# Kernel optimization log

Measured on AMD Instinct MI355X. Metric: run time of the kernel, lower is better.

The kernel has to match this reference:

```python
import jax, jax.numpy as jnp
import numpy as np
from jax import lax

V, H = 50257, 256
B, S, T = 128, 50, 32
TQ = 32


def position_encoding(emb):
    # emb: (B, S, T, H); l[s, e] = 1 - s/(T-1) - e/(H-1)*(1 - 2*s/(T-1))
    slen, elen = emb.shape[2], emb.shape[3]
    s = jnp.arange(slen, dtype=jnp.float32)[:, None] / (slen - 1)
    e = jnp.arange(elen, dtype=jnp.float32)[None, :] / (elen - 1)
    l = 1.0 - s - e * (1.0 - 2.0 * s)  # (T, H)
    return jnp.sum(emb * l[None, None], axis=2)  # (B, S, H)


def gru_seq(x, Wih, Whh, bih, bhh):
    # x: (B, T, H); torch GRU cell math; returns outputs (B,T,H), last hidden (B,H)
    h0 = jnp.zeros((x.shape[0], Whh.shape[1]), x.dtype)
    def step(h, xt):
        gi = xt @ Wih.T + bih
        gh = h @ Whh.T + bhh
        ir, iz, inn = jnp.split(gi, 3, axis=-1)
        hr, hz, hn = jnp.split(gh, 3, axis=-1)
        r = jax.nn.sigmoid(ir + hr)
        z = jax.nn.sigmoid(iz + hz)
        n = jnp.tanh(inn + r * hn)
        h_new = (1.0 - z) * n + z * h
        return h_new, h_new
    h_last, ys = lax.scan(step, h0, jnp.swapaxes(x, 0, 1))
    return jnp.swapaxes(ys, 0, 1), h_last


def setup_inputs() -> dict:
    key = jax.random.key(0)
    ks = jax.random.split(key, 16)
    def g(k, shape, scale=0.05):
        return (jax.random.normal(k, shape, dtype=jnp.float32) * scale)
    inp = {
        "contexts": jax.random.randint(ks[0], (B, S, T), 0, V, dtype=jnp.int32),
        "questions": jax.random.randint(ks[1], (B, TQ), 0, V, dtype=jnp.int32),
        "emb": jax.random.uniform(ks[2], (V, H), jnp.float32, -1.0, 1.0),
        "Wih_f": g(ks[3], (3 * H, H)), "Whh_f": g(ks[4], (3 * H, H)),
        "bih_f": jnp.zeros((3 * H,), jnp.float32), "bhh_f": jnp.zeros((3 * H,), jnp.float32),
        "Wih_b": g(ks[5], (3 * H, H)), "Whh_b": g(ks[6], (3 * H, H)),
        "bih_b": jnp.zeros((3 * H,), jnp.float32), "bhh_b": jnp.zeros((3 * H,), jnp.float32),
        "Wih_q": g(ks[7], (3 * H, H)), "Whh_q": g(ks[8], (3 * H, H)),
        "bih_q": jnp.zeros((3 * H,), jnp.float32), "bhh_q": jnp.zeros((3 * H,), jnp.float32),
        "Wo": g(ks[9], (V, H)), "bo": jnp.zeros((V,), jnp.float32),
    }
    return inp


def reference(contexts, questions, emb, Wih_f, Whh_f, bih_f, bhh_f,
              Wih_b, Whh_b, bih_b, bhh_b, Wih_q, Whh_q, bih_q, bhh_q, Wo, bo):
    # InputNet: embed -> position encoding -> bidirectional GRU (halves summed)
    ctx = emb[contexts]                      # (B, S, T, H)
    ctx = position_encoding(ctx)             # (B, S, H)  (dropout = eval no-op)
    out_f, _ = gru_seq(ctx, Wih_f, Whh_f, bih_f, bhh_f)
    out_b, _ = gru_seq(ctx[:, ::-1], Wih_b, Whh_b, bih_b, bhh_b)
    facts = out_f + out_b[:, ::-1]           # (B, S, H)
    # QuestionNet: embed -> GRU, take last hidden
    qemb = emb[questions]                    # (B, TQ, H)
    _, q = gru_seq(qemb, Wih_q, Whh_q, bih_q, bhh_q)   # (B, H)
    # AttnNet: dot-product scores + softmax over sentences (vectorized)
    energies = jnp.einsum('bsd,bd->bs', facts, q)
    attn = jax.nn.softmax(energies, axis=-1)           # (B, S)
    # memory read: bmm(attn, facts)
    read = jnp.einsum('bs,bsd->bd', attn, facts)       # (B, H)
    out = jnp.tanh(q * read) @ Wo.T + bo               # (B, V)
    return out
```

## Files before the change

### kernel.cpp

```cpp
#include <hip/hip_runtime.h>

#define V 50257
#define H 256
#define B 128
#define S 50
#define T 32
#define TQ 32

typedef __bf16 bf16x8 __attribute__((ext_vector_type(8)));
typedef float f32x4 __attribute__((ext_vector_type(4)));

__device__ inline unsigned short f2bf(float x) {
  __bf16 b = (__bf16)x;
  return __builtin_bit_cast(unsigned short, b);
}

__global__ __launch_bounds__(256) void k_wconv(
    const float* w0, const float* w1, const float* w2,
    const float* w3, const float* w4, const float* w5,
    unsigned short* dst) {
  int mat = blockIdx.x / 192;
  int blk = blockIdx.x % 192;
  const float* src = (mat == 0) ? w0 : (mat == 1) ? w1 : (mat == 2) ? w2
                   : (mat == 3) ? w3 : (mat == 4) ? w4 : w5;
  int off = blk * 1024 + threadIdx.x * 4;
  float4 v = *(const float4*)(src + off);
  unsigned short* d = dst + mat * 196608 + off;
  d[0] = f2bf(v.x); d[1] = f2bf(v.y); d[2] = f2bf(v.z); d[3] = f2bf(v.w);
}

__global__ __launch_bounds__(256) void k_embed(
    const int* ctx_idx, const int* q_idx, const float* emb,
    unsigned short* ctx_bf, unsigned short* q_bf) {
  __shared__ int sidx[T];
  int r = blockIdx.x;
  int tid = threadIdx.x;
  if (r < B * S) {
    if (tid < T) sidx[tid] = ctx_idx[r * T + tid];
    __syncthreads();
    float e = tid * (1.0f / 255.0f);
    float acc = 0.f;
    #pragma unroll 4
    for (int t = 0; t < T; ++t) {
      float tf = t * (1.0f / 31.0f);
      float w = (1.0f - tf) - e * (1.0f - 2.0f * tf);
      acc += emb[sidx[t] * H + tid] * w;
    }
    ctx_bf[r * H + tid] = f2bf(acc);
  } else {
    int rq = r - B * S;
    q_bf[rq * H + tid] = f2bf(emb[q_idx[rq] * H + tid]);
  }
}

__global__ __launch_bounds__(256) void k_gemm(
    const unsigned short* __restrict__ Xb, const unsigned short* __restrict__ Wb,
    const float* __restrict__ bias, float* __restrict__ Out) {
  const int n0 = blockIdx.x * 64;
  const int m0 = blockIdx.y * 128;
  __shared__ unsigned short lA[128 * 40];
  __shared__ unsigned short lB[64 * 40];
  int tid = threadIdx.x;
  int lane = tid & 63, wv = tid >> 6;
  int lr = lane & 15, lg = lane >> 4;
  f32x4 acc[2][4] = {};
  int sr = tid >> 2, skk = (tid & 3) * 8;
  for (int kt = 0; kt < 8; ++kt) {
    int k0 = kt * 32;
    __syncthreads();
    *(uint4*)&lA[sr * 40 + skk]        = *(const uint4*)&Xb[(m0 + sr) * 256 + k0 + skk];
    *(uint4*)&lA[(sr + 64) * 40 + skk] = *(const uint4*)&Xb[(m0 + sr + 64) * 256 + k0 + skk];
    *(uint4*)&lB[sr * 40 + skk]        = *(const uint4*)&Wb[(n0 + sr) * 256 + k0 + skk];
    __syncthreads();
    bf16x8 av0 = *(const bf16x8*)&lA[(wv * 32 + lr) * 40 + lg * 8];
    bf16x8 av1 = *(const bf16x8*)&lA[(wv * 32 + 16 + lr) * 40 + lg * 8];
    #pragma unroll
    for (int nt = 0; nt < 4; ++nt) {
      bf16x8 bv = *(const bf16x8*)&lB[(nt * 16 + lr) * 40 + lg * 8];
      acc[0][nt] = __builtin_amdgcn_mfma_f32_16x16x32_bf16(av0, bv, acc[0][nt], 0, 0, 0);
      acc[1][nt] = __builtin_amdgcn_mfma_f32_16x16x32_bf16(av1, bv, acc[1][nt], 0, 0, 0);
    }
  }
  #pragma unroll
  for (int nt = 0; nt < 4; ++nt) {
    int col = n0 + nt * 16 + lr;
    float bs = bias[col];
    #pragma unroll
    for (int mt = 0; mt < 2; ++mt) {
      #pragma unroll
      for (int r = 0; r < 4; ++r) {
        int row = m0 + wv * 32 + mt * 16 + lg * 4 + r;
        Out[row * 768 + col] = acc[mt][nt][r] + bs;
      }
    }
  }
}

__global__ __launch_bounds__(512) void k_rnn(
    const float* __restrict__ Gf, const float* __restrict__ Gb, const float* __restrict__ Gq,
    const unsigned short* __restrict__ WhF, const unsigned short* __restrict__ WhB,
    const unsigned short* __restrict__ WhQ,
    const float* __restrict__ bhF, const float* __restrict__ bhB, const float* __restrict__ bhQ,
    float* __restrict__ outF, float* __restrict__ outB, float* __restrict__ qvec) {
  int blk = blockIdx.x;
  int mode = blk >> 3;
  int rg = blk & 7;
  const float* G = (mode == 0) ? Gf : (mode == 1) ? Gb : Gq;
  const unsigned short* Wh = (mode == 0) ? WhF : (mode == 1) ? WhB : WhQ;
  const float* bh = (mode == 0) ? bhF : (mode == 1) ? bhB : bhQ;
  const int Tn = (mode == 2) ? TQ : S;
  const int SEQ = (mode == 2) ? TQ : S;
  float* ob = (mode == 0) ? outF : outB;

  __shared__ unsigned short hb[16 * 264];
  __shared__ float hf[16 * 264];

  int tid = threadIdx.x;
  for (int i = tid; i < 16 * 264; i += 512) { hb[i] = 0; hf[i] = 0.f; }
  int lane = tid & 63, wv = tid >> 6;
  int wcol = wv * 32;
  int lr = lane & 15, lg = lane >> 4;
  __syncthreads();

  for (int t = 0; t < Tn; ++t) {
    int s = (mode == 1) ? (S - 1 - t) : t;
    bf16x8 af[8];
    #pragma unroll
    for (int kt = 0; kt < 8; ++kt)
      af[kt] = *(const bf16x8*)&hb[lr * 264 + kt * 32 + lg * 8];
    __syncthreads();

    f32x4 acc[6] = {};
    #pragma unroll
    for (int g = 0; g < 3; ++g) {
      #pragma unroll
      for (int nt = 0; nt < 2; ++nt) {
        int n = g * 256 + wcol + nt * 16 + lr;
        const unsigned short* wp = Wh + n * 256 + lg * 8;
        #pragma unroll
        for (int kt = 0; kt < 8; ++kt) {
          bf16x8 bv = *(const bf16x8*)(wp + kt * 32);
          acc[g * 2 + nt] = __builtin_amdgcn_mfma_f32_16x16x32_bf16(af[kt], bv, acc[g * 2 + nt], 0, 0, 0);
        }
      }
    }
    #pragma unroll
    for (int nt = 0; nt < 2; ++nt) {
      int j = wcol + nt * 16 + lr;
      float bhr = bh[j], bhz = bh[256 + j], bhn = bh[512 + j];
      #pragma unroll
      for (int r = 0; r < 4; ++r) {
        int m = lg * 4 + r;
        int grow = ((rg * 16 + m) * SEQ + s) * 768;
        float xr = G[grow + j];
        float xz = G[grow + 256 + j];
        float xn = G[grow + 512 + j];
        float hr = acc[0 + nt][r] + bhr;
        float hz = acc[2 + nt][r] + bhz;
        float hn = acc[4 + nt][r] + bhn;
        float rgate = 1.f / (1.f + expf(-(xr + hr)));
        float zgate = 1.f / (1.f + expf(-(xz + hz)));
        float ngate = tanhf(xn + rgate * hn);
        float hold = hf[m * 264 + j];
        float hnew = (1.f - zgate) * ngate + zgate * hold;
        hf[m * 264 + j] = hnew;
        hb[m * 264 + j] = f2bf(hnew);
        if (mode == 2) {
          if (t == TQ - 1) qvec[(rg * 16 + m) * H + j] = hnew;
        } else {
          ob[((rg * 16 + m) * S + s) * H + j] = hnew;
        }
      }
    }
    __syncthreads();
  }
}

__global__ __launch_bounds__(256) void k_attn(
    const float* __restrict__ outF, const float* __restrict__ outB,
    const float* __restrict__ qvec, unsigned short* __restrict__ tqv) {
  int b = blockIdx.x, tid = threadIdx.x;
  __shared__ float fs[S * H];
  __shared__ float qs[H];
  __shared__ float es[S];
  qs[tid] = qvec[b * H + tid];
  for (int s = 0; s < S; ++s)
    fs[s * H + tid] = outF[(b * S + s) * H + tid] + outB[(b * S + s) * H + tid];
  __syncthreads();
  int lane = tid & 63, wv = tid >> 6;
  for (int s = wv; s < S; s += 4) {
    const float* fr = &fs[s * H];
    float p = 0.f;
    #pragma unroll
    for (int j = 0; j < 4; ++j) p += fr[lane * 4 + j] * qs[lane * 4 + j];
    #pragma unroll
    for (int off = 32; off > 0; off >>= 1) p += __shfl_xor(p, off, 64);
    if (lane == 0) es[s] = p;
  }
  __syncthreads();
  float mx = -1e30f;
  for (int s = 0; s < S; ++s) mx = fmaxf(mx, es[s]);
  float sum = 0.f;
  for (int s = 0; s < S; ++s) sum += expf(es[s] - mx);
  float inv = 1.f / sum;
  float rd = 0.f;
  for (int s = 0; s < S; ++s) rd += expf(es[s] - mx) * inv * fs[s * H + tid];
  tqv[b * H + tid] = f2bf(tanhf(qs[tid] * rd));
}

__global__ __launch_bounds__(256) void k_out(
    const unsigned short* __restrict__ tqv, const float* __restrict__ Wo,
    const float* __restrict__ bo, float* __restrict__ Out) {
  int n0 = blockIdx.x * 64;
  int tid = threadIdx.x, lane = tid & 63, wv = tid >> 6;
  int lr = lane & 15, lg = lane >> 4;
  __shared__ unsigned short lA[B * H];
  #pragma unroll
  for (int i = 0; i < 16; ++i) {
    int c = tid + i * 256;
    int row = c >> 5, kk = (c & 31) * 8;
    int dst = row * 512 + ((kk * 2) ^ ((row & 7) << 4));
    *(uint4*)((char*)lA + dst) = *(const uint4*)&tqv[row * H + kk];
  }
  __syncthreads();
  int vcol = n0 + wv * 16 + lr;
  int vc = (vcol < V) ? vcol : (V - 1);
  f32x4 acc[8] = {};
  for (int kt = 0; kt < 8; ++kt) {
    const float* wp = &Wo[vc * H + kt * 32 + lg * 8];
    float4 w0 = *(const float4*)wp;
    float4 w1 = *(const float4*)(wp + 4);
    bf16x8 bv;
    bv[0] = (__bf16)w0.x; bv[1] = (__bf16)w0.y; bv[2] = (__bf16)w0.z; bv[3] = (__bf16)w0.w;
    bv[4] = (__bf16)w1.x; bv[5] = (__bf16)w1.y; bv[6] = (__bf16)w1.z; bv[7] = (__bf16)w1.w;
    #pragma unroll
    for (int mt = 0; mt < 8; ++mt) {
      int row = mt * 16 + lr;
      int boff = row * 512 + ((kt * 64 + lg * 16) ^ ((row & 7) << 4));
      bf16x8 av = *(const bf16x8*)((const char*)lA + boff);
      acc[mt] = __builtin_amdgcn_mfma_f32_16x16x32_bf16(av, bv, acc[mt], 0, 0, 0);
    }
  }
  if (vcol < V) {
    float bs = bo[vcol];
    #pragma unroll
    for (int mt = 0; mt < 8; ++mt)
      #pragma unroll
      for (int r = 0; r < 4; ++r) {
        int row = mt * 16 + lg * 4 + r;
        Out[row * V + vcol] = acc[mt][r] + bs;
      }
  }
}

extern "C" void kernel_launch(void* const* d_in, const int* in_sizes, int n_in,
                              void* d_out, int out_size, void* d_ws, size_t ws_size,
                              hipStream_t stream) {
  const int* contexts  = (const int*)d_in[0];
  const int* questions = (const int*)d_in[1];
  const float* emb   = (const float*)d_in[2];
  const float* Wih_f = (const float*)d_in[3];
  const float* Whh_f = (const float*)d_in[4];
  const float* bih_f = (const float*)d_in[5];
  const float* bhh_f = (const float*)d_in[6];
  const float* Wih_b = (const float*)d_in[7];
  const float* Whh_b = (const float*)d_in[8];
  const float* bih_b = (const float*)d_in[9];
  const float* bhh_b = (const float*)d_in[10];
  const float* Wih_q = (const float*)d_in[11];
  const float* Whh_q = (const float*)d_in[12];
  const float* bih_q = (const float*)d_in[13];
  const float* bhh_q = (const float*)d_in[14];
  const float* Wo = (const float*)d_in[15];
  const float* bo = (const float*)d_in[16];
  float* out = (float*)d_out;

  char* ws = (char*)d_ws;
  unsigned short* ctx_bf = (unsigned short*)(ws);
  unsigned short* q_bf   = (unsigned short*)(ws + 3276800);
  unsigned short* wbf    = (unsigned short*)(ws + 5373952);
  unsigned short* WihF_b = wbf + 0 * 196608;
  unsigned short* WhhF_b = wbf + 1 * 196608;
  unsigned short* WihB_b = wbf + 2 * 196608;
  unsigned short* WhhB_b = wbf + 3 * 196608;
  unsigned short* WihQ_b = wbf + 4 * 196608;
  unsigned short* WhhQ_b = wbf + 5 * 196608;
  float* Gf   = (float*)(ws + 7733248);
  float* Gb   = (float*)(ws + 27394048);
  float* Gq   = (float*)(ws + 47054848);
  float* outFp = (float*)(ws + 59637760);
  float* outBp = (float*)(ws + 66191360);
  float* qvec = (float*)(ws + 72744960);
  unsigned short* tqv = (unsigned short*)(ws + 72876032);

  k_wconv<<<1152, 256, 0, stream>>>(Wih_f, Whh_f, Wih_b, Whh_b, Wih_q, Whh_q, wbf);
  k_embed<<<B * S + B * TQ, 256, 0, stream>>>(contexts, questions, emb, ctx_bf, q_bf);
  k_gemm<<<dim3(12, 50), 256, 0, stream>>>(ctx_bf, WihF_b, bih_f, Gf);
  k_gemm<<<dim3(12, 50), 256, 0, stream>>>(ctx_bf, WihB_b, bih_b, Gb);
  k_gemm<<<dim3(12, 32), 256, 0, stream>>>(q_bf, WihQ_b, bih_q, Gq);
  k_rnn<<<24, 512, 0, stream>>>(Gf, Gb, Gq, WhhF_b, WhhB_b, WhhQ_b,
                                bhh_f, bhh_b, bhh_q, outFp, outBp, qvec);
  k_attn<<<B, 256, 0, stream>>>(outFp, outBp, qvec, tqv);
  k_out<<<786, 256, 0, stream>>>(tqv, Wo, bo, out);
}
```

Baseline: 532.6 us.

## Keep GRU recurrent weights and hidden state in registers; vectorize embedding gather

The GRU kernel now loads its slice of the recurrent weight matrix and the hidden-bias values into registers once, instead of re-reading them from global memory on every timestep. The float hidden state also lives in registers rather than shared memory, and the gates use exp2-based sigmoid and tanh approximations. The embedding kernel now gives each wavefront one row, reads float4 vectors and broadcasts indices by shuffle, so it launches a quarter as many blocks. The catch is heavy register pressure (48 bf16x8 weight fragments per thread), which could spill, plus slightly different rounding from the fast transcendental functions.

```diff
diff --git a/kernel.cpp b/kernel.cpp
--- a/kernel.cpp
+++ b/kernel.cpp
@@ -13,6 +13,13 @@
 __device__ inline unsigned short f2bf(float x) {
   __bf16 b = (__bf16)x;
   return __builtin_bit_cast(unsigned short, b);
+}
+
+__device__ inline float sigf(float x) {
+  return 1.f / (1.f + __builtin_amdgcn_exp2f(-1.4426950408889634f * x));
+}
+__device__ inline float tanhfast(float x) {
+  return 1.f - 2.f / (__builtin_amdgcn_exp2f(2.8853900817779268f * x) + 1.f);
 }
 
 __global__ __launch_bounds__(256) void k_wconv(
@@ -30,26 +37,39 @@
 }
 
 __global__ __launch_bounds__(256) void k_embed(
-    const int* ctx_idx, const int* q_idx, const float* emb,
-    unsigned short* ctx_bf, unsigned short* q_bf) {
-  __shared__ int sidx[T];
-  int r = blockIdx.x;
+    const int* __restrict__ ctx_idx, const int* __restrict__ q_idx,
+    const float* __restrict__ emb,
+    unsigned short* __restrict__ ctx_bf, unsigned short* __restrict__ q_bf) {
   int tid = threadIdx.x;
+  int wv = tid >> 6, lane = tid & 63;
+  int r = blockIdx.x * 4 + wv;
   if (r < B * S) {
-    if (tid < T) sidx[tid] = ctx_idx[r * T + tid];
-    __syncthreads();
-    float e = tid * (1.0f / 255.0f);
-    float acc = 0.f;
+    int myidx = ctx_idx[r * T + (lane & 31)];
+    float e0 = (float)(lane * 4) * (1.f / 255.f);
+    float4 acc = make_float4(0.f, 0.f, 0.f, 0.f);
     #pragma unroll 4
     for (int t = 0; t < T; ++t) {
-      float tf = t * (1.0f / 31.0f);
-      float w = (1.0f - tf) - e * (1.0f - 2.0f * tf);
-      acc += emb[sidx[t] * H + tid] * w;
-    }
-    ctx_bf[r * H + tid] = f2bf(acc);
+      int id = __shfl(myidx, t, 64);
+      float4 v = *(const float4*)&emb[(long)id * H + lane * 4];
+      float tf = t * (1.f / 31.f);
+      float a = 1.f - tf;
+      float bb = 2.f * tf - 1.f;
+      acc.x += (a + (e0 + 0.f * (1.f / 255.f)) * bb) * v.x;
+      acc.y += (a + (e0 + 1.f * (1.f / 255.f)) * bb) * v.y;
+      acc.z += (a + (e0 + 2.f * (1.f / 255.f)) * bb) * v.z;
+      acc.w += (a + (e0 + 3.f * (1.f / 255.f)) * bb) * v.w;
+    }
+    ushort4 o;
+    o.x = f2bf(acc.x); o.y = f2bf(acc.y); o.z = f2bf(acc.z); o.w = f2bf(acc.w);
+    *(ushort4*)&ctx_bf[r * H + lane * 4] = o;
   } else {
     int rq = r - B * S;
-    q_bf[rq * H + tid] = f2bf(emb[q_idx[rq] * H + tid]);
+    if (rq < B * TQ) {
+      float4 v = *(const float4*)&emb[(long)q_idx[rq] * H + lane * 4];
+      ushort4 o;
+      o.x = f2bf(v.x); o.y = f2bf(v.y); o.z = f2bf(v.z); o.w = f2bf(v.w);
+      *(ushort4*)&q_bf[rq * H + lane * 4] = o;
+    }
   }
 }
 
@@ -96,7 +116,7 @@
   }
 }
 
-__global__ __launch_bounds__(512) void k_rnn(
+__global__ __launch_bounds__(512, 2) void k_rnn(
     const float* __restrict__ Gf, const float* __restrict__ Gb, const float* __restrict__ Gq,
     const unsigned short* __restrict__ WhF, const unsigned short* __restrict__ WhB,
     const unsigned short* __restrict__ WhQ,
@@ -109,70 +129,92 @@
   const unsigned short* Wh = (mode == 0) ? WhF : (mode == 1) ? WhB : WhQ;
   const float* bh = (mode == 0) ? bhF : (mode == 1) ? bhB : bhQ;
   const int Tn = (mode == 2) ? TQ : S;
-  const int SEQ = (mode == 2) ? TQ : S;
+  const int SEQ = Tn;
   float* ob = (mode == 0) ? outF : outB;
 
   __shared__ unsigned short hb[16 * 264];
-  __shared__ float hf[16 * 264];
 
   int tid = threadIdx.x;
-  for (int i = tid; i < 16 * 264; i += 512) { hb[i] = 0; hf[i] = 0.f; }
   int lane = tid & 63, wv = tid >> 6;
-  int wcol = wv * 32;
   int lr = lane & 15, lg = lane >> 4;
+
+  for (int i = tid; i < 16 * 264; i += 512) hb[i] = 0;
+
+  bf16x8 w[3][2][8];
+  #pragma unroll
+  for (int g = 0; g < 3; ++g)
+    #pragma unroll
+    for (int nt = 0; nt < 2; ++nt) {
+      const unsigned short* wp = Wh + (g * 256 + wv * 32 + nt * 16 + lr) * 256 + lg * 8;
+      #pragma unroll
+      for (int kt = 0; kt < 8; ++kt)
+        w[g][nt][kt] = *(const bf16x8*)(wp + kt * 32);
+    }
+
+  float bhv[3][2];
+  #pragma unroll
+  for (int g = 0; g < 3; ++g)
+    #pragma unroll
+    for (int nt = 0; nt < 2; ++nt)
+      bhv[g][nt] = bh[g * 256 + wv * 32 + nt * 16 + lr];
+
+  float hcur[2][4] = {};
+
   __syncthreads();
 
   for (int t = 0; t < Tn; ++t) {
     int s = (mode == 1) ? (S - 1 - t) : t;
-    bf16x8 af[8];
-    #pragma unroll
-    for (int kt = 0; kt < 8; ++kt)
-      af[kt] = *(const bf16x8*)&hb[lr * 264 + kt * 32 + lg * 8];
-    __syncthreads();
-
     f32x4 acc[6] = {};
     #pragma unroll
-    for (int g = 0; g < 3; ++g) {
-      #pragma unroll
-      for (int nt = 0; nt < 2; ++nt) {
-        int n = g * 256 + wcol + nt * 16 + lr;
-        const unsigned short* wp = Wh + n * 256 + lg * 8;
-        #pragma unroll
-        for (int kt = 0; kt < 8; ++kt) {
-          bf16x8 bv = *(const bf16x8*)(wp + kt * 32);
-          acc[g * 2 + nt] = __builtin_amdgcn_mfma_f32_16x16x32_bf16(af[kt], bv, acc[g * 2 + nt], 0, 0, 0);
-        }
+    for (int kt = 0; kt < 8; ++kt) {
+      bf16x8 a = *(const bf16x8*)&hb[lr * 264 + kt * 32 + lg * 8];
+      #pragma unroll
+      for (int g = 0; g < 3; ++g) {
+        acc[g * 2 + 0] = __builtin_amdgcn_mfma_f32_16x16x32_bf16(a, w[g][0][kt], acc[g * 2 + 0], 0, 0, 0);
+        acc[g * 2 + 1] = __builtin_amdgcn_mfma_f32_16x16x32_bf16(a, w[g][1][kt], acc[g * 2 + 1], 0, 0, 0);
       }
     }
     #pragma unroll
     for (int nt = 0; nt < 2; ++nt) {
-      int j = wcol + nt * 16 + lr;
-      float bhr = bh[j], bhz = bh[256 + j], bhn = bh[512 + j];
+      int j = wv * 32 + nt * 16 + lr;
       #pragma unroll
       for (int r = 0; r < 4; ++r) {
         int m = lg * 4 + r;
-        int grow = ((rg * 16 + m) * SEQ + s) * 768;
+        long grow = (long)((rg * 16 + m) * SEQ + s) * 768;
         float xr = G[grow + j];
         float xz = G[grow + 256 + j];
         float xn = G[grow + 512 + j];
-        float hr = acc[0 + nt][r] + bhr;
-        float hz = acc[2 + nt][r] + bhz;
-        float hn = acc[4 + nt][r] + bhn;
-        float rgate = 1.f / (1.f + expf(-(xr + hr)));
-        float zgate = 1.f / (1.f + expf(-(xz + hz)));
-        float ngate = tanhf(xn + rgate * hn);
-        float hold = hf[m * 264 + j];
-        float hnew = (1.f - zgate) * ngate + zgate * hold;
-        hf[m * 264 + j] = hnew;
-        hb[m * 264 + j] = f2bf(hnew);
-        if (mode == 2) {
-          if (t == TQ - 1) qvec[(rg * 16 + m) * H + j] = hnew;
-        } else {
-          ob[((rg * 16 + m) * S + s) * H + j] = hnew;
-        }
+        float rr = sigf(xr + acc[0 + nt][r] + bhv[0][nt]);
+        float zz = sigf(xz + acc[2 + nt][r] + bhv[1][nt]);
+        float nn = tanhfast(xn + rr * (acc[4 + nt][r] + bhv[2][nt]));
+        hcur[nt][r] = (1.f - zz) * nn + zz * hcur[nt][r];
       }
     }
     __syncthreads();
+    #pragma unroll
+    for (int nt = 0; nt < 2; ++nt) {
+      int j = wv * 32 + nt * 16 + lr;
+      #pragma unroll
+      for (int r = 0; r < 4; ++r) {
+        int m = lg * 4 + r;
+        hb[m * 264 + j] = f2bf(hcur[nt][r]);
+        if (mode != 2)
+          ob[(long)((rg * 16 + m) * S + s) * H + j] = hcur[nt][r];
+      }
+    }
+    __syncthreads();
+  }
+
+  if (mode == 2) {
+    #pragma unroll
+    for (int nt = 0; nt < 2; ++nt) {
+      int j = wv * 32 + nt * 16 + lr;
+      #pragma unroll
+      for (int r = 0; r < 4; ++r) {
+        int m = lg * 4 + r;
+        qvec[(rg * 16 + m) * H + j] = hcur[nt][r];
+      }
+    }
   }
 }
 
@@ -294,7 +336,7 @@
   unsigned short* tqv = (unsigned short*)(ws + 72876032);
 
   k_wconv<<<1152, 256, 0, stream>>>(Wih_f, Whh_f, Wih_b, Whh_b, Wih_q, Whh_q, wbf);
-  k_embed<<<B * S + B * TQ, 256, 0, stream>>>(contexts, questions, emb, ctx_bf, q_bf);
+  k_embed<<<(B * S + B * TQ + 3) / 4, 256, 0, stream>>>(contexts, questions, emb, ctx_bf, q_bf);
   k_gemm<<<dim3(12, 50), 256, 0, stream>>>(ctx_bf, WihF_b, bih_f, Gf);
   k_gemm<<<dim3(12, 50), 256, 0, stream>>>(ctx_bf, WihB_b, bih_b, Gb);
   k_gemm<<<dim3(12, 32), 256, 0, stream>>>(q_bf, WihQ_b, bih_q, Gq);
```

New measurement: 485.2 us. 8.9% less time.
